# Kernel tuning notes

Measured on AMD Instinct MI355X. Metric: run time of the kernel, lower is better.

Reference implementation:

```python
import jax, jax.numpy as jnp
import numpy as np

NETWORK_MAP = {'DMN': [34, 35, 66, 67, 64, 65, 22, 23, 24, 25], 'SMN': [0, 1, 56, 57, 68, 69], 'VN': [42, 43, 44, 45, 46, 47, 48, 49, 50, 51, 52, 53], 'SN': [28, 29, 30, 31, 32, 33], 'FPN': [6, 7, 58, 59, 60, 61], 'LN': [36, 37, 38, 39, 40, 41], 'VAN': [10, 11, 14, 15], 'BGN': [70, 71, 72, 73, 74, 75, 76, 77], 'CereN': list(range(90, 116))}
N, K, B, IN_DIM, HID, HEADS = 116, 9, 512, 123, 128, 4
FLAT = K * HID + HID  # 1280


def _pool_mat():
    P = np.zeros((N, K), np.float32)
    for k, idxs in enumerate(NETWORK_MAP.values()):
        P[np.array(idxs), k] = 1.0
    return jnp.asarray(P)


def _bn(x, g, b, m, v):
    # eval-mode BatchNorm1d with running stats
    return (x - m) / jnp.sqrt(v + 1e-5) * g + b


def _gat(h, adj, W, a, g, bt, m, v):
    Bb, Nn, _ = h.shape
    H = a.shape[0]
    D = a.shape[1] // 2  # head_dim
    Wh = (h @ W).reshape(Bb, Nn, H, D)
    # additive GAT score factorization: (cat([Wh_i, Wh_j]) * a).sum(-1) = ei + ej
    ei = jnp.einsum('bnhd,hd->bnh', Wh, a[:, :D])
    ej = jnp.einsum('bnhd,hd->bnh', Wh, a[:, D:])
    e = ei[:, :, None, :] + ej[:, None, :, :]          # [B,N,N,H]
    e = jnp.where(e > 0, e, 0.2 * e)                   # leaky_relu(0.2)
    e = jnp.where((adj == 0)[..., None], -jnp.inf, e)  # mask non-edges
    attn = jax.nn.softmax(e, axis=2)                   # over neighbors j
    out = jnp.einsum('bijh,bjhd->bihd', attn, Wh).reshape(Bb, Nn, -1)
    out = _bn(out, g, bt, m, v)
    return jax.nn.elu(out) + h @ W


def setup_inputs() -> dict:
    key = jax.random.key(0)
    ks = jax.random.split(key, 24)
    f32 = jnp.float32

    def lin(k, fi, fo):
        return jax.random.normal(k, (fi, fo), f32) / np.sqrt(fi)

    x = jax.random.normal(ks[0], (B, N, IN_DIM), f32)
    adj = jax.random.randint(ks[1], (B, N, N), 0, 2).astype(f32)
    adj = jnp.maximum(adj, jnp.eye(N, dtype=f32)[None])  # self-loops
    return {
        'x': x, 'adj': adj,
        'W_enc': lin(ks[2], IN_DIM, HID), 'b_enc': jnp.zeros((HID,), f32),
        'bn_in_g': 1.0 + 0.1 * jax.random.normal(ks[3], (HID,), f32),
        'bn_in_b': 0.1 * jax.random.normal(ks[4], (HID,), f32),
        'bn_in_m': 0.05 * jax.random.normal(ks[5], (HID,), f32),
        'bn_in_v': jax.random.uniform(ks[6], (HID,), f32, 0.5, 1.5),
        'vne': 0.02 * jax.random.normal(ks[7], (1, 1, HID), f32),
        'W1': lin(ks[8], HID, HID),
        'a1': 0.1 * jax.random.normal(ks[9], (HEADS, 2 * (HID // HEADS)), f32),
        'g1': 1.0 + 0.1 * jax.random.normal(ks[10], (HID,), f32),
        'bt1': 0.1 * jax.random.normal(ks[11], (HID,), f32),
        'm1': 0.05 * jax.random.normal(ks[12], (HID,), f32),
        'v1': jax.random.uniform(ks[13], (HID,), f32, 0.5, 1.5),
        'W2': lin(ks[14], HID, HID),
        'a2': 0.1 * jax.random.normal(ks[15], (HEADS, 2 * (HID // HEADS)), f32),
        'g2': 1.0 + 0.1 * jax.random.normal(ks[16], (HID,), f32),
        'bt2': 0.1 * jax.random.normal(ks[17], (HID,), f32),
        'm2': 0.05 * jax.random.normal(ks[18], (HID,), f32),
        'v2': jax.random.uniform(ks[19], (HID,), f32, 0.5, 1.5),
        'Wv': lin(ks[20], 2 * HID, HID), 'bv': jnp.zeros((HID,), f32),
        'pool_mat': _pool_mat(),
        'Wa1': lin(ks[21], HID, 32), 'ba1': jnp.zeros((32,), f32),
        'Wa2': lin(ks[22], 32, 1), 'ba2': jnp.zeros((1,), f32),
        'ln_g': jnp.ones((FLAT,), f32), 'ln_b': jnp.zeros((FLAT,), f32),
        'Wc1': lin(ks[23], FLAT, 256), 'bc1': jnp.zeros((256,), f32),
        'Wc2': lin(jax.random.fold_in(key, 99), 256, 2), 'bc2': jnp.zeros((2,), f32),
    }


def reference(x, adj, W_enc, b_enc, bn_in_g, bn_in_b, bn_in_m, bn_in_v, vne,
              W1, a1, g1, bt1, m1, v1, W2, a2, g2, bt2, m2, v2,
              Wv, bv, pool_mat, Wa1, ba1, Wa2, ba2, ln_g, ln_b,
              Wc1, bc1, Wc2, bc2):
    Bb = x.shape[0]
    h = jax.nn.elu(x @ W_enc + b_enc)                 # node_encoder (dropout=eval)
    h = _bn(h, bn_in_g, bn_in_b, bn_in_m, bn_in_v)
    vn = vne + h.mean(axis=1, keepdims=True)          # [B,1,HID]
    h = _gat(h, adj, W1, a1, g1, bt1, m1, v1)
    vn_new = jax.nn.elu(jnp.concatenate([vn, h.mean(axis=1, keepdims=True)], -1) @ Wv + bv)
    h = h + vn_new * 0.1
    h2 = _gat(h, adj, W2, a2, g2, bt2, m2, v2)
    h = h2 + h
    vn = jax.nn.elu(jnp.concatenate([vn_new, h.mean(axis=1, keepdims=True)], -1) @ Wv + bv)
    pooled = jnp.einsum('bnd,nk->bkd', h, pool_mat)   # virtual-network pooling [B,K,HID]
    s = jnp.tanh(pooled @ Wa1 + ba1) @ Wa2 + ba2      # [B,K,1]
    net_w = jax.nn.softmax(s, axis=1)
    pooled = pooled * net_w
    flat = jnp.concatenate([pooled.reshape(Bb, -1), vn[:, 0]], axis=1)  # [B,FLAT]
    mu = flat.mean(axis=-1, keepdims=True)
    var = flat.var(axis=-1, keepdims=True)
    flat = (flat - mu) / jnp.sqrt(var + 1e-5) * ln_g + ln_b  # LayerNorm
    logits = jax.nn.elu(flat @ Wc1 + bc1) @ Wc2 + bc2        # classifier (dropout=eval)
    return (logits, flat)
```

## Files before the change

kernel.cpp:

```cpp
#include <hip/hip_runtime.h>
#include <hip/hip_bf16.h>
#include <math.h>

#define BATCH 512
#define N_NODES 116
#define IN_DIM 123
#define HID 128
#define HEADS 4
#define FLAT_DIM 1280

static constexpr int BN_TOT = BATCH * N_NODES;
static constexpr int HROW = N_NODES * HID;

typedef short short8 __attribute__((ext_vector_type(8)));
typedef float f32x16 __attribute__((ext_vector_type(16)));

__device__ __forceinline__ float elu1(float x) {
    return x > 0.f ? x : __expf(x) - 1.f;
}
__device__ __forceinline__ short bfb(float x) {
    __hip_bfloat16 b = __float2bfloat16(x);
    return *reinterpret_cast<short*>(&b);
}
__device__ __forceinline__ float bf2f(short s) {
    return __bfloat162float(*reinterpret_cast<__hip_bfloat16*>(&s));
}

__global__ __launch_bounds__(256) void prep_all(
    const float* __restrict__ x, const float* __restrict__ adj,
    const float* __restrict__ W_enc,
    const float* __restrict__ W1, const float* __restrict__ a1,
    const float* __restrict__ W2, const float* __restrict__ a2,
    short* __restrict__ xb, unsigned int* __restrict__ adjp,
    short* __restrict__ Wencb,
    short* __restrict__ Wt1, short* __restrict__ We1,
    short* __restrict__ Wt2, short* __restrict__ We2)
{
    const int blk = blockIdx.x, t = threadIdx.x;
    if (blk < 128) {
        const float* W = (blk < 64) ? W1 : W2;
        const float* a = (blk < 64) ? a1 : a2;
        short* Wt = (blk < 64) ? Wt1 : Wt2;
        short* We = (blk < 64) ? We1 : We2;
        const int idx = (blk & 63) * 256 + t;
        const int h = idx >> 12, nn = (idx >> 7) & 31, k = idx & 127;
        Wt[idx] = bfb(W[k * HID + h * 32 + nn]);
        short wv = 0;
        if (nn < 2) {
            const float* ap = a + h * 64 + nn * 32;
            float s = 0.f;
#pragma unroll 8
            for (int d = 0; d < 32; ++d) s += W[k * HID + h * 32 + d] * ap[d];
            wv = bfb(s);
        }
        We[idx] = wv;
    } else if (blk < 192) {
        const int idx = (blk - 128) * 256 + t;
        const int col = idx >> 7, k = idx & 127;
        Wencb[idx] = (k < IN_DIM) ? bfb(W_enc[(size_t)k * HID + col]) : (short)0;
    } else if (blk < 192 + BN_TOT / 4) {
        const int row = (blk - 192) * 4 + (t >> 6);
        const int l = t & 63;
        const float v1 = adj[(size_t)row * N_NODES + l];
        const float v2 = (l < N_NODES - 64) ? adj[(size_t)row * N_NODES + 64 + l] : 0.f;
        const unsigned long long m1 = __ballot(v1 != 0.f);
        const unsigned long long m2 = __ballot(v2 != 0.f);
        if (l == 0) {
            uint4 v;
            v.x = (unsigned int)m1; v.y = (unsigned int)(m1 >> 32);
            v.z = (unsigned int)m2; v.w = (unsigned int)(m2 >> 32);
            *reinterpret_cast<uint4*>(&adjp[(size_t)row * 4]) = v;
        }
    } else {
        const int i = (blk - (192 + BN_TOT / 4)) * 256 + t;
        const int row = i >> 4, kb = (i & 15) * 8;
        short8 v;
#pragma unroll
        for (int e = 0; e < 8; ++e) {
            const int k = kb + e;
            v[e] = (k < IN_DIM) ? bfb(x[(size_t)row * IN_DIM + k]) : (short)0;
        }
        *reinterpret_cast<short8*>(&xb[(size_t)row * 128 + kb]) = v;
    }
}

__global__ __launch_bounds__(256) void wc1prep_kernel(
    const float* __restrict__ Wc1, short* __restrict__ wc1t)
{
    const int idx = blockIdx.x * 256 + threadIdx.x;
    const int k = idx >> 8, n = idx & 255;
    wc1t[(size_t)n * FLAT_DIM + k] = bfb(Wc1[(size_t)k * 256 + n]);
}

__global__ __launch_bounds__(256) void enc_mfma(
    const short* __restrict__ xb, const short* __restrict__ Wencb,
    const float* __restrict__ bias,
    const float* __restrict__ g, const float* __restrict__ bta,
    const float* __restrict__ mn, const float* __restrict__ vr,
    short* __restrict__ houtb)
{
    const int t = threadIdx.x;
    const int lane = t & 63, w = t >> 6;
    const int half = lane >> 5, nn = lane & 31;
    const int row0 = blockIdx.x * 128 + w * 32;
    const short8* ap = reinterpret_cast<const short8*>(xb + (size_t)(row0 + nn) * 128);
    short8 af[8];
#pragma unroll
    for (int s = 0; s < 8; ++s) af[s] = ap[s * 2 + half];
#pragma unroll
    for (int ct = 0; ct < 4; ++ct) {
        const int col = ct * 32 + nn;
        const short8* bp = reinterpret_cast<const short8*>(Wencb + (size_t)col * 128);
        f32x16 acc = {};
#pragma unroll
        for (int s = 0; s < 8; ++s)
            acc = __builtin_amdgcn_mfma_f32_32x32x16_bf16(af[s], bp[s * 2 + half], acc, 0, 0, 0);
        const float bb = bias[col];
        const float gg = g[col], bbn = bta[col], mm = mn[col];
        const float rstd = rsqrtf(vr[col] + 1e-5f);
#pragma unroll
        for (int reg = 0; reg < 16; ++reg) {
            const int r = (reg & 3) + 8 * (reg >> 2) + 4 * half;
            float val = elu1(acc[reg] + bb);
            val = (val - mm) * rstd * gg + bbn;
            houtb[(size_t)(row0 + r) * HID + col] = bfb(val);
        }
    }
}

__global__ __launch_bounds__(128) void vn0_kernel(
    const short* __restrict__ hb, const float* __restrict__ vne,
    float* __restrict__ vn)
{
    const int b = blockIdx.x, f = threadIdx.x;
    float s = 0.f;
    for (int n = 0; n < N_NODES; ++n)
        s += bf2f(hb[(size_t)(b * N_NODES + n) * HID + f]);
    vn[b * HID + f] = vne[f] + s * (1.f / N_NODES);
}

template <int L>
__global__ __launch_bounds__(256, 4) void gat_fused(
    const short* __restrict__ hbin, short* __restrict__ houtb,
    const short* __restrict__ Wt, const short* __restrict__ Weij,
    const unsigned int* __restrict__ adjp,
    const float* __restrict__ g_, const float* __restrict__ bt_,
    const float* __restrict__ mn_, const float* __restrict__ vr_,
    const float* __restrict__ vn, const float* __restrict__ wcorr,
    const float* __restrict__ eicorr, float* __restrict__ premean)
{
    constexpr int KP = 136;
    constexpr int WP = 33;
    __shared__ __align__(16) __hip_bfloat16 s_p[N_NODES][KP];
    __shared__ __align__(16) __hip_bfloat16 s_whsb[128][WP];
    __shared__ float s_eir[232];

    const int t = threadIdx.x;
    const int n_ = blockIdx.x;
    const int b = (n_ & 7) * 64 + (n_ >> 5);
    const int h = (n_ >> 3) & 3;

    const int lane = t & 63, w = t >> 6;
    const int half = lane >> 5, nn = lane & 31;
    const int row = w * 32 + nn;
    const int hr = (row < N_NODES) ? row : 0;

    float wc = 0.f, eic = 0.f, ejc = 0.f;
    if (L == 1) {
        wc = wcorr[(size_t)b * HID + h * 32 + nn];
        eic = eicorr[b * 8 + h * 2];
        ejc = eicorr[b * 8 + h * 2 + 1];
    }

    {
        const short8* ap = reinterpret_cast<const short8*>(
            hbin + (size_t)(b * N_NODES + hr) * HID);
        const short8* wtp = reinterpret_cast<const short8*>(Wt + ((h * 32 + nn) << 7));
        const short8* wep = reinterpret_cast<const short8*>(Weij + ((h * 32 + nn) << 7));
        f32x16 wacc = {};
        f32x16 eacc = {};
#pragma unroll
        for (int s = 0; s < 8; ++s) {
            const int fi = s * 2 + half;
            const short8 af = ap[fi];
            wacc = __builtin_amdgcn_mfma_f32_32x32x16_bf16(af, wtp[fi], wacc, 0, 0, 0);
            eacc = __builtin_amdgcn_mfma_f32_32x32x16_bf16(af, wep[fi], eacc, 0, 0, 0);
        }
#pragma unroll
        for (int reg = 0; reg < 16; ++reg) {
            const int r = (reg & 3) + 8 * (reg >> 2) + 4 * half;
            s_whsb[w * 32 + r][nn] = __float2bfloat16(wacc[reg]);
        }
        if (nn == 0) {
#pragma unroll
            for (int reg = 0; reg < 16; ++reg) {
                const int r = w * 32 + (reg & 3) + 8 * (reg >> 2) + 4 * half;
                if (r < N_NODES) s_eir[r] = eacc[reg] + eic;
            }
        }
        if (nn == 1) {
#pragma unroll
            for (int reg = 0; reg < 16; ++reg) {
                const int r = w * 32 + (reg & 3) + 8 * (reg >> 2) + 4 * half;
                if (r < N_NODES) s_eir[N_NODES + r] = eacc[reg] + ejc;
            }
        }
    }
    __syncthreads();

    {
        const int l = lane;
        const float ejl = s_eir[N_NODES + l];
        const bool up = (l < N_NODES - 64);
        const float ejl2 = up ? s_eir[N_NODES + l + 64] : 0.f;
        const int i0 = w * 32;
        const uint4* ap = reinterpret_cast<const uint4*>(
            adjp + ((size_t)b * N_NODES + i0) * 4);
        auto body = [&](int ii) {
            const int i = i0 + ii;
            const uint4 aw = ap[ii];
            const float eii = s_eir[i];
            const unsigned int w1 = (l & 32) ? aw.y : aw.x;
            const unsigned int w2 = (l & 32) ? aw.w : aw.z;
            const bool bit1 = (w1 >> (l & 31)) & 1;
            const bool bit2 = (w2 >> (l & 31)) & 1;
            float e1 = eii + ejl;
            e1 = e1 > 0.f ? e1 : 0.2f * e1;
            const float x1 = bit1 ? __expf(e1) : 0.f;
            float x2 = 0.f;
            if (up) {
                float e2 = eii + ejl2;
                e2 = e2 > 0.f ? e2 : 0.2f * e2;
                x2 = bit2 ? __expf(e2) : 0.f;
            }
            s_p[i][l] = __float2bfloat16(x1);
            s_p[i][l + 64] = __float2bfloat16(x2);
        };
        if (w < 3) {
#pragma unroll 8
            for (int ii = 0; ii < 32; ++ii) body(ii);
        } else {
#pragma unroll 5
            for (int ii = 0; ii < 20; ++ii) body(ii);
        }
    }

    float psum = 0.f;
    {
        f32x16 acc = {};
        f32x16 accs = {};
        short8 ones;
#pragma unroll
        for (int e = 0; e < 8; ++e) ones[e] = (short)0x3F80;
#pragma unroll
        for (int s = 0; s < 8; ++s) {
            const int k0 = s * 16 + half * 8;
            const short8 afrag = *reinterpret_cast<const short8*>(
                &s_p[0][0] + (size_t)row * KP + k0);
            short8 bfrag;
#pragma unroll
            for (int e = 0; e < 8; ++e)
                bfrag[e] = *reinterpret_cast<const short*>(&s_whsb[k0 + e][nn]);
            acc = __builtin_amdgcn_mfma_f32_32x32x16_bf16(afrag, bfrag, acc, 0, 0, 0);
            accs = __builtin_amdgcn_mfma_f32_32x32x16_bf16(afrag, ones, accs, 0, 0, 0);
        }
        const int f = h * 32 + nn;
        const float G = g_[f], B = bt_[f], M = mn_[f];
        const float R = rsqrtf(vr_[f] + 1e-5f);
        const float vadd = (L == 1) ? 0.1f * vn[(size_t)b * HID + f] : 0.f;
#pragma unroll
        for (int reg = 0; reg < 16; ++reg) {
            const int r = (reg & 3) + 8 * (reg >> 2) + 4 * half;
            const int i = w * 32 + r;
            if (i < N_NODES) {
                const size_t off = ((size_t)b * N_NODES + i) * HID + f;
                const float aval = acc[reg] / accs[reg] + wc;
                float xv = elu1((aval - M) * R * G + B);
                float outv = xv + bf2f(*reinterpret_cast<const short*>(&s_whsb[i][nn])) + wc;
                if (L == 1) outv += bf2f(hbin[off]) + vadd;
                houtb[off] = bfb(outv);
                psum += outv;
            }
        }
    }
    psum += __shfl_xor(psum, 32);
    __syncthreads();
    if (half == 0) s_eir[w * 32 + nn] = psum;
    __syncthreads();
    if (t < 32) {
        const float s = s_eir[t] + s_eir[32 + t] + s_eir[64 + t] + s_eir[96 + t];
        premean[(size_t)b * HID + h * 32 + t] = s * (1.f / N_NODES);
    }
}

__global__ __launch_bounds__(128) void vn_mlp_kernel(
    const float* __restrict__ prev, const float* __restrict__ premean,
    const float* __restrict__ Wv, const float* __restrict__ bv,
    const float* __restrict__ W2, const float* __restrict__ a2,
    float* __restrict__ vout, float* __restrict__ wcorr,
    float* __restrict__ eicorr)
{
    __shared__ float cat[2 * HID];
    const int b = blockIdx.x, f = threadIdx.x;
    cat[f] = prev[b * HID + f];
    cat[HID + f] = premean[b * HID + f];
    __syncthreads();
    float acc = bv[f];
    for (int k = 0; k < 2 * HID; ++k) acc += cat[k] * Wv[k * HID + f];
    const float o = elu1(acc);
    vout[b * HID + f] = o;
    __syncthreads();
    cat[f] = o;
    __syncthreads();
    float wcf = 0.f;
#pragma unroll 4
    for (int k = 0; k < HID; ++k) wcf += cat[k] * W2[k * HID + f];
    wcf *= 0.1f;
    wcorr[(size_t)b * HID + f] = wcf;
    __syncthreads();
    cat[f] = wcf;
    __syncthreads();
    if (f < 8) {
        const int h = f >> 1, sel = f & 1;
        float e = 0.f;
#pragma unroll 8
        for (int d = 0; d < 32; ++d)
            e += cat[h * 32 + d] * a2[h * 64 + sel * 32 + d];
        eicorr[b * 8 + f] = e;
    }
}

__global__ __launch_bounds__(128) void pool_flat_kernel(
    const short* __restrict__ hb, const float* __restrict__ vnn,
    const float* __restrict__ pms2,
    const float* __restrict__ Wv, const float* __restrict__ bv,
    const float* __restrict__ pm,
    const float* __restrict__ Wa1, const float* __restrict__ ba1,
    const float* __restrict__ Wa2, const float* __restrict__ ba2,
    const float* __restrict__ ln_g, const float* __restrict__ ln_b,
    float* __restrict__ out, short* __restrict__ flatb)
{
    __shared__ float s_pm[N_NODES * 9];
    __shared__ float s_v[2 * HID];
    __shared__ float s_p[9][HID];
    __shared__ float s_s[9];
    __shared__ float s_red[4];
    const int b = blockIdx.x, f = threadIdx.x;
    for (int idx = f; idx < N_NODES * 9; idx += 128) s_pm[idx] = pm[idx];
    s_v[f] = vnn[b * HID + f];
    s_v[HID + f] = pms2[b * HID + f];
    __syncthreads();
    float vacc = bv[f];
    for (int k = 0; k < 2 * HID; ++k) vacc += s_v[k] * Wv[k * HID + f];
    const float vnf_f = elu1(vacc);
    float p[9] = {};
    for (int n = 0; n < N_NODES; ++n) {
        const float hv = bf2f(hb[(size_t)b * HROW + n * HID + f]);
#pragma unroll
        for (int k = 0; k < 9; ++k) p[k] += s_pm[n * 9 + k] * hv;
    }
#pragma unroll
    for (int k = 0; k < 9; ++k) s_p[k][f] = p[k];
    __syncthreads();
    for (int pass = 0; pass < 3; ++pass) {
        const int k = pass * 4 + (f >> 5);
        if (k < 9) {
            const int j = f & 31;
            float z = ba1[j];
            for (int d = 0; d < HID; ++d) z += s_p[k][d] * Wa1[d * 32 + j];
            z = tanhf(z);
            float part = z * Wa2[j];
#pragma unroll
            for (int off = 16; off; off >>= 1) part += __shfl_xor(part, off);
            if (j == 0) s_s[k] = part + ba2[0];
        }
    }
    __syncthreads();
    float smax = -1e30f;
#pragma unroll
    for (int k = 0; k < 9; ++k) smax = fmaxf(smax, s_s[k]);
    float wgt[9], ssum = 0.f;
#pragma unroll
    for (int k = 0; k < 9; ++k) { wgt[k] = expf(s_s[k] - smax); ssum += wgt[k]; }
    const float sinv = 1.f / ssum;
    float vals[10];
#pragma unroll
    for (int k = 0; k < 9; ++k) vals[k] = p[k] * wgt[k] * sinv;
    vals[9] = vnf_f;
    float lsum = 0.f, lsq = 0.f;
#pragma unroll
    for (int q = 0; q < 10; ++q) { lsum += vals[q]; lsq += vals[q] * vals[q]; }
#pragma unroll
    for (int off = 32; off; off >>= 1) {
        lsum += __shfl_xor(lsum, off);
        lsq += __shfl_xor(lsq, off);
    }
    const int lane = f & 63, wid = f >> 6;
    if (lane == 0) { s_red[wid * 2] = lsum; s_red[wid * 2 + 1] = lsq; }
    __syncthreads();
    const float tot = s_red[0] + s_red[2];
    const float totsq = s_red[1] + s_red[3];
    const float mean = tot * (1.f / FLAT_DIM);
    const float var = totsq * (1.f / FLAT_DIM) - mean * mean;
    const float rstd = rsqrtf(var + 1e-5f);
    float* fout = out + 1024 + (size_t)b * FLAT_DIM;
    short* fb = flatb + (size_t)b * FLAT_DIM;
#pragma unroll
    for (int k = 0; k < 9; ++k) {
        const int j = k * HID + f;
        const float v = (vals[k] - mean) * rstd * ln_g[j] + ln_b[j];
        fout[j] = v;
        fb[j] = bfb(v);
    }
    const int j = 9 * HID + f;
    const float v9 = (vals[9] - mean) * rstd * ln_g[j] + ln_b[j];
    fout[j] = v9;
    fb[j] = bfb(v9);
}

__global__ __launch_bounds__(64) void cls_mm_kernel(
    const short* __restrict__ flatb, const short* __restrict__ wc1t,
    const float* __restrict__ bc1, float* __restrict__ hid)
{
    const int lane = threadIdx.x;
    const int half = lane >> 5, nn = lane & 31;
    const int mt = blockIdx.x >> 3;
    const int ct = blockIdx.x & 7;
    const int r0 = mt * 32;
    const int c0 = ct * 32;
    const short8* ap = reinterpret_cast<const short8*>(flatb + (size_t)(r0 + nn) * FLAT_DIM);
    const short8* bp = reinterpret_cast<const short8*>(wc1t + (size_t)(c0 + nn) * FLAT_DIM);
    f32x16 acc = {};
#pragma unroll 8
    for (int s = 0; s < 80; ++s) {
        const int fi = s * 2 + half;
        acc = __builtin_amdgcn_mfma_f32_32x32x16_bf16(ap[fi], bp[fi], acc, 0, 0, 0);
    }
    const float bb = bc1[c0 + nn];
#pragma unroll
    for (int reg = 0; reg < 16; ++reg) {
        const int row = (reg & 3) + 8 * (reg >> 2) + 4 * half;
        hid[(size_t)(r0 + row) * 256 + c0 + nn] = elu1(acc[reg] + bb);
    }
}

__global__ __launch_bounds__(256) void logits_kernel(
    const float* __restrict__ hid, const float* __restrict__ Wc2,
    const float* __restrict__ bc2, float* __restrict__ out)
{
    const int idx = blockIdx.x * 256 + threadIdx.x;
    const int row = idx >> 1, c = idx & 1;
    const float4* hp = reinterpret_cast<const float4*>(hid + (size_t)row * 256);
    float acc = 0.f;
#pragma unroll 8
    for (int q = 0; q < 64; ++q) {
        const float4 hv = hp[q];
        acc += hv.x * Wc2[(q * 4 + 0) * 2 + c] + hv.y * Wc2[(q * 4 + 1) * 2 + c]
             + hv.z * Wc2[(q * 4 + 2) * 2 + c] + hv.w * Wc2[(q * 4 + 3) * 2 + c];
    }
    out[idx] = acc + bc2[c];
}

extern "C" void kernel_launch(void* const* d_in, const int* in_sizes, int n_in,
                              void* d_out, int out_size, void* d_ws, size_t ws_size,
                              hipStream_t stream)
{
    const float* x     = (const float*)d_in[0];
    const float* adj   = (const float*)d_in[1];
    const float* W_enc = (const float*)d_in[2];
    const float* b_enc = (const float*)d_in[3];
    const float* bn_g  = (const float*)d_in[4];
    const float* bn_b  = (const float*)d_in[5];
    const float* bn_m  = (const float*)d_in[6];
    const float* bn_v  = (const float*)d_in[7];
    const float* vne   = (const float*)d_in[8];
    const float* W1    = (const float*)d_in[9];
    const float* a1    = (const float*)d_in[10];
    const float* g1    = (const float*)d_in[11];
    const float* bt1   = (const float*)d_in[12];
    const float* m1    = (const float*)d_in[13];
    const float* v1    = (const float*)d_in[14];
    const float* W2    = (const float*)d_in[15];
    const float* a2    = (const float*)d_in[16];
    const float* g2    = (const float*)d_in[17];
    const float* bt2   = (const float*)d_in[18];
    const float* m2    = (const float*)d_in[19];
    const float* v2    = (const float*)d_in[20];
    const float* Wv    = (const float*)d_in[21];
    const float* bv    = (const float*)d_in[22];
    const float* pm    = (const float*)d_in[23];
    const float* Wa1   = (const float*)d_in[24];
    const float* ba1   = (const float*)d_in[25];
    const float* Wa2   = (const float*)d_in[26];
    const float* ba2   = (const float*)d_in[27];
    const float* ln_g  = (const float*)d_in[28];
    const float* ln_b  = (const float*)d_in[29];
    const float* Wc1   = (const float*)d_in[30];
    const float* bc1   = (const float*)d_in[31];
    const float* Wc2   = (const float*)d_in[32];
    const float* bc2   = (const float*)d_in[33];
    float* out = (float*)d_out;

    char* ws = (char*)d_ws;
    short* xb    = (short*)ws;
    short* flatb = (short*)ws;
    short* wc1t  = flatb + (size_t)BATCH * FLAT_DIM;
    float* hid   = (float*)(wc1t + 256 * FLAT_DIM);
    short* hb0  = (short*)(ws + (size_t)BN_TOT * HID * 4);
    short* h1b  = hb0 + (size_t)BN_TOT * HID;
    float* tail = (float*)(h1b + (size_t)BN_TOT * HID);
    float* vn0g = tail;
    float* vnn  = vn0g + BATCH * HID;
    float* pms1 = vnn + BATCH * HID;
    float* pms2 = pms1 + BATCH * HID;
    float* wcorr = pms2 + BATCH * HID;
    float* eicorr = wcorr + BATCH * HID;
    unsigned int* adjp = (unsigned int*)(eicorr + BATCH * 8);
    short* Wt1  = (short*)(adjp + (size_t)BN_TOT * 4);
    short* We1  = Wt1 + 16384;
    short* Wt2  = We1 + 16384;
    short* We2  = Wt2 + 16384;
    short* Wencb = We2 + 16384;

    const int prep_blocks = 192 + BN_TOT / 4 + (BN_TOT * 16) / 256;
    prep_all<<<prep_blocks, 256, 0, stream>>>(x, adj, W_enc, W1, a1, W2, a2,
                                              xb, adjp, Wencb, Wt1, We1, Wt2, We2);
    enc_mfma<<<BN_TOT / 128, 256, 0, stream>>>(xb, Wencb, b_enc, bn_g, bn_b,
                                               bn_m, bn_v, hb0);
    vn0_kernel<<<BATCH, 128, 0, stream>>>(hb0, vne, vn0g);
    gat_fused<0><<<BATCH * HEADS, 256, 0, stream>>>(
        hb0, h1b, Wt1, We1, adjp, g1, bt1, m1, v1,
        nullptr, nullptr, nullptr, pms1);
    vn_mlp_kernel<<<BATCH, 128, 0, stream>>>(vn0g, pms1, Wv, bv, W2, a2,
                                             vnn, wcorr, eicorr);
    gat_fused<1><<<BATCH * HEADS, 256, 0, stream>>>(
        h1b, hb0, Wt2, We2, adjp, g2, bt2, m2, v2,
        vnn, wcorr, eicorr, pms2);
    wc1prep_kernel<<<1280, 256, 0, stream>>>(Wc1, wc1t);
    pool_flat_kernel<<<BATCH, 128, 0, stream>>>(hb0, vnn, pms2, Wv, bv, pm,
                                                Wa1, ba1, Wa2, ba2,
                                                ln_g, ln_b, out, flatb);
    cls_mm_kernel<<<128, 64, 0, stream>>>(flatb, wc1t, bc1, hid);
    logits_kernel<<<4, 256, 0, stream>>>(hid, Wc2, bc2, out);
}
```

Baseline: 211.0 us.

## Transpose Wh tile in LDS with XOR swizzle and pack P writes

Stores the per-head Wh tile transposed in LDS with an XOR swizzle, so the B-fragment of the attention MFMA becomes one 16-byte load instead of eight scalar strided loads. The exponent stage now has each lane handle two adjacent neighbours and writes them as one packed bf16 pair with v_cvt_pk_bf16_f32, replacing two scalar stores per row. The softmax division becomes a hardware reciprocal multiply, and the Wc1 transpose is folded into the prep kernel to save one launch. The reciprocal is slightly less precise, and the swizzle and packing change how the LDS banks are used.

Result: faster. 193.5 us (median of 2 runs) (-8.3%).

```diff
diff --git a/kernel.cpp b/kernel.cpp
--- a/kernel.cpp
+++ b/kernel.cpp
@@ -28,13 +28,14 @@
 
 __global__ __launch_bounds__(256) void prep_all(
     const float* __restrict__ x, const float* __restrict__ adj,
-    const float* __restrict__ W_enc,
+    const float* __restrict__ W_enc, const float* __restrict__ Wc1,
     const float* __restrict__ W1, const float* __restrict__ a1,
     const float* __restrict__ W2, const float* __restrict__ a2,
     short* __restrict__ xb, unsigned int* __restrict__ adjp,
     short* __restrict__ Wencb,
     short* __restrict__ Wt1, short* __restrict__ We1,
-    short* __restrict__ Wt2, short* __restrict__ We2)
+    short* __restrict__ Wt2, short* __restrict__ We2,
+    short* __restrict__ wc1t)
 {
     const int blk = blockIdx.x, t = threadIdx.x;
     if (blk < 128) {
@@ -71,7 +72,7 @@
             v.z = (unsigned int)m2; v.w = (unsigned int)(m2 >> 32);
             *reinterpret_cast<uint4*>(&adjp[(size_t)row * 4]) = v;
         }
-    } else {
+    } else if (blk < 192 + BN_TOT / 4 + (BN_TOT * 16) / 256) {
         const int i = (blk - (192 + BN_TOT / 4)) * 256 + t;
         const int row = i >> 4, kb = (i & 15) * 8;
         short8 v;
@@ -81,15 +82,11 @@
             v[e] = (k < IN_DIM) ? bfb(x[(size_t)row * IN_DIM + k]) : (short)0;
         }
         *reinterpret_cast<short8*>(&xb[(size_t)row * 128 + kb]) = v;
-    }
-}
-
-__global__ __launch_bounds__(256) void wc1prep_kernel(
-    const float* __restrict__ Wc1, short* __restrict__ wc1t)
-{
-    const int idx = blockIdx.x * 256 + threadIdx.x;
-    const int k = idx >> 8, n = idx & 255;
-    wc1t[(size_t)n * FLAT_DIM + k] = bfb(Wc1[(size_t)k * 256 + n]);
+    } else {
+        const int idx = (blk - (192 + BN_TOT / 4 + (BN_TOT * 16) / 256)) * 256 + t;
+        const int k = idx >> 8, n = idx & 255;
+        wc1t[(size_t)n * FLAT_DIM + k] = bfb(Wc1[(size_t)k * 256 + n]);
+    }
 }
 
 __global__ __launch_bounds__(256) void enc_mfma(
@@ -150,9 +147,8 @@
     const float* __restrict__ eicorr, float* __restrict__ premean)
 {
     constexpr int KP = 136;
-    constexpr int WP = 33;
     __shared__ __align__(16) __hip_bfloat16 s_p[N_NODES][KP];
-    __shared__ __align__(16) __hip_bfloat16 s_whsb[128][WP];
+    __shared__ __align__(16) __hip_bfloat16 s_whsT[32][128];
     __shared__ float s_eir[232];
 
     const int t = threadIdx.x;
@@ -164,6 +160,7 @@
     const int half = lane >> 5, nn = lane & 31;
     const int row = w * 32 + nn;
     const int hr = (row < N_NODES) ? row : 0;
+    const int swz = (nn & 7) << 4;
 
     float wc = 0.f, eic = 0.f, ejc = 0.f;
     if (L == 1) {
@@ -186,10 +183,13 @@
             wacc = __builtin_amdgcn_mfma_f32_32x32x16_bf16(af, wtp[fi], wacc, 0, 0, 0);
             eacc = __builtin_amdgcn_mfma_f32_32x32x16_bf16(af, wep[fi], eacc, 0, 0, 0);
         }
+        char* wbase = reinterpret_cast<char*>(&s_whsT[0][0]) + nn * 256;
 #pragma unroll
         for (int reg = 0; reg < 16; ++reg) {
             const int r = (reg & 3) + 8 * (reg >> 2) + 4 * half;
-            s_whsb[w * 32 + r][nn] = __float2bfloat16(wacc[reg]);
+            const int col = w * 32 + r;
+            *reinterpret_cast<__hip_bfloat16*>(wbase + ((col * 2) ^ swz)) =
+                __float2bfloat16(wacc[reg]);
         }
         if (nn == 0) {
 #pragma unroll
@@ -210,38 +210,33 @@
 
     {
         const int l = lane;
-        const float ejl = s_eir[N_NODES + l];
-        const bool up = (l < N_NODES - 64);
-        const float ejl2 = up ? s_eir[N_NODES + l + 64] : 0.f;
+        const int c0 = 2 * l;
+        const bool valid = (c0 < N_NODES);
+        const float ejl  = valid ? s_eir[N_NODES + c0] : 0.f;
+        const float ejl2 = valid ? s_eir[N_NODES + c0 + 1] : 0.f;
+        const int sh = c0 & 31;
         const int i0 = w * 32;
+        const int cnt = (w < 3) ? 32 : 20;
         const uint4* ap = reinterpret_cast<const uint4*>(
             adjp + ((size_t)b * N_NODES + i0) * 4);
-        auto body = [&](int ii) {
-            const int i = i0 + ii;
+        char* prow0 = reinterpret_cast<char*>(&s_p[i0][0]) + c0 * 2;
+#pragma unroll 4
+        for (int ii = 0; ii < cnt; ++ii) {
             const uint4 aw = ap[ii];
-            const float eii = s_eir[i];
-            const unsigned int w1 = (l & 32) ? aw.y : aw.x;
-            const unsigned int w2 = (l & 32) ? aw.w : aw.z;
-            const bool bit1 = (w1 >> (l & 31)) & 1;
-            const bool bit2 = (w2 >> (l & 31)) & 1;
+            const unsigned int wa = (l & 16) ? aw.y : aw.x;
+            const unsigned int wb = (l & 16) ? aw.w : aw.z;
+            const unsigned int word = (l & 32) ? wb : wa;
+            const unsigned int bits = word >> sh;
+            const float eii = s_eir[i0 + ii];
             float e1 = eii + ejl;
-            e1 = e1 > 0.f ? e1 : 0.2f * e1;
-            const float x1 = bit1 ? __expf(e1) : 0.f;
-            float x2 = 0.f;
-            if (up) {
-                float e2 = eii + ejl2;
-                e2 = e2 > 0.f ? e2 : 0.2f * e2;
-                x2 = bit2 ? __expf(e2) : 0.f;
-            }
-            s_p[i][l] = __float2bfloat16(x1);
-            s_p[i][l + 64] = __float2bfloat16(x2);
-        };
-        if (w < 3) {
-#pragma unroll 8
-            for (int ii = 0; ii < 32; ++ii) body(ii);
-        } else {
-#pragma unroll 5
-            for (int ii = 0; ii < 20; ++ii) body(ii);
+            float e2 = eii + ejl2;
+            e1 = fmaxf(e1, 0.2f * e1);
+            e2 = fmaxf(e2, 0.2f * e2);
+            const float x1 = ((bits & 1) && valid) ? __expf(e1) : 0.f;
+            const float x2 = ((bits & 2) && valid) ? __expf(e2) : 0.f;
+            unsigned int pk;
+            asm("v_cvt_pk_bf16_f32 %0, %1, %2" : "=v"(pk) : "v"(x1), "v"(x2));
+            *reinterpret_cast<unsigned int*>(prow0 + ii * (KP * 2)) = pk;
         }
     }
 
@@ -252,15 +247,14 @@
         short8 ones;
 #pragma unroll
         for (int e = 0; e < 8; ++e) ones[e] = (short)0x3F80;
+        const char* wbase = reinterpret_cast<const char*>(&s_whsT[0][0]) + nn * 256;
 #pragma unroll
         for (int s = 0; s < 8; ++s) {
             const int k0 = s * 16 + half * 8;
             const short8 afrag = *reinterpret_cast<const short8*>(
                 &s_p[0][0] + (size_t)row * KP + k0);
-            short8 bfrag;
-#pragma unroll
-            for (int e = 0; e < 8; ++e)
-                bfrag[e] = *reinterpret_cast<const short*>(&s_whsb[k0 + e][nn]);
+            const short8 bfrag = *reinterpret_cast<const short8*>(
+                wbase + ((k0 * 2) ^ swz));
             acc = __builtin_amdgcn_mfma_f32_32x32x16_bf16(afrag, bfrag, acc, 0, 0, 0);
             accs = __builtin_amdgcn_mfma_f32_32x32x16_bf16(afrag, ones, accs, 0, 0, 0);
         }
@@ -268,15 +262,18 @@
         const float G = g_[f], B = bt_[f], M = mn_[f];
         const float R = rsqrtf(vr_[f] + 1e-5f);
         const float vadd = (L == 1) ? 0.1f * vn[(size_t)b * HID + f] : 0.f;
+        const char* wrb = reinterpret_cast<const char*>(&s_whsT[0][0]) + nn * 256;
 #pragma unroll
         for (int reg = 0; reg < 16; ++reg) {
             const int r = (reg & 3) + 8 * (reg >> 2) + 4 * half;
             const int i = w * 32 + r;
             if (i < N_NODES) {
                 const size_t off = ((size_t)b * N_NODES + i) * HID + f;
-                const float aval = acc[reg] / accs[reg] + wc;
+                const float aval = acc[reg] * __builtin_amdgcn_rcpf(accs[reg]) + wc;
                 float xv = elu1((aval - M) * R * G + B);
-                float outv = xv + bf2f(*reinterpret_cast<const short*>(&s_whsb[i][nn])) + wc;
+                const float res = bf2f(*reinterpret_cast<const short*>(
+                    wrb + ((i * 2) ^ swz)));
+                float outv = xv + res + wc;
                 if (L == 1) outv += bf2f(hbin[off]) + vadd;
                 houtb[off] = bfb(outv);
                 psum += outv;
@@ -504,8 +501,6 @@
     char* ws = (char*)d_ws;
     short* xb    = (short*)ws;
     short* flatb = (short*)ws;
-    short* wc1t  = flatb + (size_t)BATCH * FLAT_DIM;
-    float* hid   = (float*)(wc1t + 256 * FLAT_DIM);
     short* hb0  = (short*)(ws + (size_t)BN_TOT * HID * 4);
     short* h1b  = hb0 + (size_t)BN_TOT * HID;
     float* tail = (float*)(h1b + (size_t)BN_TOT * HID);
@@ -521,10 +516,13 @@
     short* Wt2  = We1 + 16384;
     short* We2  = Wt2 + 16384;
     short* Wencb = We2 + 16384;
-
-    const int prep_blocks = 192 + BN_TOT / 4 + (BN_TOT * 16) / 256;
-    prep_all<<<prep_blocks, 256, 0, stream>>>(x, adj, W_enc, W1, a1, W2, a2,
-                                              xb, adjp, Wencb, Wt1, We1, Wt2, We2);
+    short* wc1t = Wencb + 16384;
+    float* hid  = (float*)(wc1t + 256 * FLAT_DIM);
+
+    const int prep_blocks = 192 + BN_TOT / 4 + (BN_TOT * 16) / 256 + 1280;
+    prep_all<<<prep_blocks, 256, 0, stream>>>(x, adj, W_enc, Wc1, W1, a1, W2, a2,
+                                              xb, adjp, Wencb, Wt1, We1, Wt2, We2,
+                                              wc1t);
     enc_mfma<<<BN_TOT / 128, 256, 0, stream>>>(xb, Wencb, b_enc, bn_g, bn_b,
                                                bn_m, bn_v, hb0);
     vn0_kernel<<<BATCH, 128, 0, stream>>>(hb0, vne, vn0g);
@@ -536,7 +534,6 @@
     gat_fused<1><<<BATCH * HEADS, 256, 0, stream>>>(
         h1b, hb0, Wt2, We2, adjp, g2, bt2, m2, v2,
         vnn, wcorr, eicorr, pms2);
-    wc1prep_kernel<<<1280, 256, 0, stream>>>(Wc1, wc1t);
     pool_flat_kernel<<<BATCH, 128, 0, stream>>>(hb0, vnn, pms2, Wv, bv, pm,
                                                 Wa1, ba1, Wa2, ba2,
                                                 ln_g, ln_b, out, flatb);
```
